# Performance work log

Hardware: AMD Instinct MI355X
Metric: run time of the kernel (lower is better)

## Reference

```python
import jax, jax.numpy as jnp
import numpy as np

B, S, D = 4, 2048, 768
H = 12
HD = D // H  # 64


def setup_inputs() -> dict:
    key = jax.random.key(0)
    k1, k2, k3 = jax.random.split(key, 3)
    x = jax.random.normal(k1, (B, S, D), dtype=jnp.float32)
    w_qkv = jax.random.normal(k2, (D, 3 * D), dtype=jnp.float32) * (1.0 / np.sqrt(D))
    b_qkv = jnp.zeros((3 * D,), dtype=jnp.float32)
    w_proj = jax.random.normal(k3, (D, D), dtype=jnp.float32) * (1.0 / np.sqrt(D))
    b_proj = jnp.zeros((D,), dtype=jnp.float32)
    return {"x": x, "w_qkv": w_qkv, "b_qkv": b_qkv, "w_proj": w_proj, "b_proj": b_proj}


def reference(x, w_qkv, b_qkv, w_proj, b_proj):
    b, s, d = x.shape
    qkv = x @ w_qkv + b_qkv                      # [B,S,3D]
    q, k, v = jnp.split(qkv, 3, axis=-1)
    # [B,S,D] -> [B,H,S,HD]
    q = q.reshape(b, s, H, HD).transpose(0, 2, 1, 3)
    k = k.reshape(b, s, H, HD).transpose(0, 2, 1, 3)
    v = v.reshape(b, s, H, HD).transpose(0, 2, 1, 3)
    scores = jnp.einsum("bhqd,bhkd->bhqk", q, k) / jnp.sqrt(jnp.float32(HD))
    causal = jnp.tril(jnp.ones((s, s), dtype=bool))
    scores = jnp.where(causal[None, None, :, :], scores, jnp.float32(-jnp.inf))
    attn = jax.nn.softmax(scores, axis=-1)       # dropout p=0.0 -> identity
    out = jnp.einsum("bhqk,bhkd->bhqd", attn, v)  # [B,H,S,HD]
    out = out.transpose(0, 2, 1, 3).reshape(b, s, d)
    return out @ w_proj + b_proj
```

## Files before the change

kernel.cpp:

```cpp
#include <hip/hip_runtime.h>
#include <hip/hip_bf16.h>

typedef __hip_bfloat16 bf16;
typedef __bf16 bf16x8 __attribute__((ext_vector_type(8)));
typedef float f32x4 __attribute__((ext_vector_type(4)));

#define MFMA(a, b, c) __builtin_amdgcn_mfma_f32_16x16x32_bf16(a, b, c, 0, 0, 0)
#define EXP2F(x) __builtin_exp2f(x)

constexpr int Bn = 4, Sn = 2048, Dn = 768, Hn = 12;
constexpr int N3 = 3 * Dn;
constexpr int Mrows = Bn * Sn;

constexpr size_t XB_OFF    = 0;
constexpr size_t WQKV_OFF  = 12582912;
constexpr size_t WPROJ_OFF = 16121856;
constexpr size_t Q_OFF     = 17301504;
constexpr size_t K_OFF     = 29884416;
constexpr size_t VT_OFF    = 42467328;
constexpr size_t O_OFF     = 55050240;

#define QSCALE 0.1803368801111243f

__device__ __forceinline__ void gload16(const void* g, void* l) {
  __builtin_amdgcn_global_load_lds((__attribute__((address_space(1))) void*)g,
                                   (__attribute__((address_space(3))) void*)l,
                                   16, 0, 0);
}

__device__ __forceinline__ unsigned int cvt_pk_bf16(float lo, float hi) {
  unsigned int r;
  asm("v_cvt_pk_bf16_f32 %0, %1, %2" : "=v"(r) : "v"(lo), "v"(hi));
  return r;
}

__global__ __launch_bounds__(256) void cvt_x_kernel(const float* __restrict__ in,
                                                    bf16* __restrict__ out, int n4) {
  int i = blockIdx.x * 256 + threadIdx.x;
  if (i >= n4) return;
  float4 f = reinterpret_cast<const float4*>(in)[i];
  uint2 o;
  o.x = cvt_pk_bf16(f.x, f.y);
  o.y = cvt_pk_bf16(f.z, f.w);
  reinterpret_cast<uint2*>(out)[i] = o;
}

__global__ __launch_bounds__(256) void transpose_cvt(const float* __restrict__ in,
                                                     bf16* __restrict__ out, int K, int N) {
  __shared__ float tile[32][33];
  int n0 = blockIdx.x * 32, k0 = blockIdx.y * 32;
  int tx = threadIdx.x & 31, ty = threadIdx.x >> 5;
  for (int r = ty; r < 32; r += 8)
    tile[r][tx] = in[(size_t)(k0 + r) * N + n0 + tx];
  __syncthreads();
  for (int r = ty; r < 32; r += 8)
    out[(size_t)(n0 + r) * K + k0 + tx] = __float2bfloat16(tile[tx][r]);
}

__global__ __launch_bounds__(256) void gemm_qkv(const bf16* __restrict__ A,
                                                const bf16* __restrict__ BT,
                                                const float* __restrict__ bias,
                                                bf16* __restrict__ Qo,
                                                bf16* __restrict__ Ko,
                                                bf16* __restrict__ Vt) {
  __shared__ __align__(16) bf16 As[2][128 * 32];
  __shared__ __align__(16) bf16 Bs[2][128 * 32];
  const int tid = threadIdx.x;
  const int m0 = blockIdx.x * 128, n0 = blockIdx.y * 128;
  const int w = tid >> 6, lane = tid & 63;
  const int wr = w >> 1, wc = w & 1;
  const int lr = lane & 15, lg = lane >> 4;

  f32x4 acc[4][4] = {};

  auto stage = [&](int k0, int sb) {
    for (int r = 0; r < 2; ++r) {
      int c = tid + r * 256;
      int row = c >> 2, ch = c & 3;
      int gch = ch ^ ((row >> 1) & 3);
      gload16(A + (size_t)(m0 + row) * Dn + k0 + gch * 8, &As[sb][c * 8]);
      gload16(BT + (size_t)(n0 + row) * Dn + k0 + gch * 8, &Bs[sb][c * 8]);
    }
  };

  stage(0, 0);
  __syncthreads();

  const int sw = (lr >> 1) & 3;
  const int aoff = (wr * 64 + lr) * 32 + ((lg ^ sw) << 3);
  const int boff = (wc * 64 + lr) * 32 + ((lg ^ sw) << 3);
  int buf = 0;

  for (int kt = 0; kt < 24; ++kt) {
    if (kt < 23) stage((kt + 1) * 32, buf ^ 1);
    bf16x8 af[4], bfr[4];
    for (int mi = 0; mi < 4; ++mi)
      af[mi] = *reinterpret_cast<const bf16x8*>(&As[buf][aoff + mi * 512]);
    for (int ni = 0; ni < 4; ++ni)
      bfr[ni] = *reinterpret_cast<const bf16x8*>(&Bs[buf][boff + ni * 512]);
    for (int mi = 0; mi < 4; ++mi)
      for (int ni = 0; ni < 4; ++ni)
        acc[mi][ni] = MFMA(af[mi], bfr[ni], acc[mi][ni]);
    __syncthreads();
    buf ^= 1;
  }

  for (int ni = 0; ni < 4; ++ni) {
    const int col = n0 + wc * 64 + ni * 16 + lr;
    const float bv = bias[col];
    const int seg = (col >= Dn) + (col >= 2 * Dn);
    const int d = col - seg * Dn;
    const int h = d >> 6, hd = d & 63;
    for (int mi = 0; mi < 4; ++mi) {
      f32x4 v = acc[mi][ni];
      const int row0 = m0 + wr * 64 + mi * 16 + lg * 4;
      const int b = row0 >> 11, s0 = row0 & 2047;
      const size_t bh = (size_t)(b * Hn + h);
      if (seg == 2) {
        uint2 pk;
        pk.x = cvt_pk_bf16(v[0] + bv, v[1] + bv);
        pk.y = cvt_pk_bf16(v[2] + bv, v[3] + bv);
        *reinterpret_cast<uint2*>(&Vt[(bh * 64 + hd) * Sn + s0]) = pk;
      } else if (seg == 0) {
        for (int r = 0; r < 4; ++r)
          Qo[(bh * Sn + s0 + r) * 64 + hd] = __float2bfloat16((v[r] + bv) * QSCALE);
      } else {
        for (int r = 0; r < 4; ++r)
          Ko[(bh * Sn + s0 + r) * 64 + hd] = __float2bfloat16(v[r] + bv);
      }
    }
  }
}

__global__ __launch_bounds__(512) void attn_fwd(const bf16* __restrict__ Q,
                                                const bf16* __restrict__ K,
                                                const bf16* __restrict__ Vt,
                                                bf16* __restrict__ O) {
  __shared__ __align__(16) bf16 Ks[2][64 * 64];
  __shared__ __align__(16) bf16 Vs[2][64 * 64];
  __shared__ __align__(16) bf16 Ps[8][16 * 64];
  const int tid = threadIdx.x, w = tid >> 6, lane = tid & 63;
  const int lr = lane & 15, lg = lane >> 4;
  const int bid = blockIdx.x;
  const int pt = bid / 48;
  const int qt = (pt < 8) ? (15 - 2 * pt) : (2 * pt - 16);
  const int bh = bid % 48;
  const int q0 = qt * 128;
  const size_t base = (size_t)bh * Sn * 64;
  const int wrow = q0 + w * 16;

  bf16x8 qf[2];
  for (int kk = 0; kk < 2; ++kk)
    qf[kk] = *reinterpret_cast<const bf16x8*>(
        Q + base + (size_t)(wrow + lr) * 64 + kk * 32 + lg * 8);

  f32x4 o[4] = {};
  f32x4 lacc = {};

  const int nt = 2 * qt + 2;

  const int r0 = tid >> 3, s0w = (tid & 7) ^ (r0 & 7);
  const bf16* kp = K + base + r0 * 64 + s0w * 8;
  const bf16* vp = Vt + base + (size_t)r0 * Sn + s0w * 8;

  gload16(kp, &Ks[0][tid * 8]);
  gload16(vp, &Vs[0][tid * 8]);
  kp += 4096; vp += 64;
  __syncthreads();

  int buf = 0;
  for (int t = 0; t < nt; ++t) {
    if (t + 1 < nt) {
      const int sb = buf ^ 1;
      gload16(kp, &Ks[sb][tid * 8]);
      gload16(vp, &Vs[sb][tid * 8]);
      kp += 4096; vp += 64;
    }

    if (t * 64 <= wrow + 15) {
      f32x4 sf[4];
      __builtin_amdgcn_s_setprio(1);
      for (int ni = 0; ni < 4; ++ni) {
        const int krow = ni * 16 + lr;
        bf16x8 kf0 = *reinterpret_cast<const bf16x8*>(&Ks[buf][krow * 64 + (lg ^ (lr & 7)) * 8]);
        bf16x8 kf1 = *reinterpret_cast<const bf16x8*>(&Ks[buf][krow * 64 + ((4 + lg) ^ (lr & 7)) * 8]);
        f32x4 z = {};
        z = MFMA(kf0, qf[0], z);
        z = MFMA(kf1, qf[1], z);
        sf[ni] = z;
      }
      __builtin_amdgcn_s_setprio(0);
      if (t * 64 + 63 > wrow) {
        const int qg = wrow + lr;
        for (int ni = 0; ni < 4; ++ni)
          for (int r = 0; r < 4; ++r) {
            int kg = t * 64 + ni * 16 + lg * 4 + r;
            if (kg > qg) sf[ni][r] = -1e30f;
          }
      }
      for (int ni = 0; ni < 4; ++ni) {
        f32x4 z = sf[ni];
        z[0] = EXP2F(z[0]);
        z[1] = EXP2F(z[1]);
        z[2] = EXP2F(z[2]);
        z[3] = EXP2F(z[3]);
        sf[ni] = z;
        lacc += z;
      }
      for (int ni = 0; ni < 4; ++ni) {
        const int chunk = ni * 2 + (lg >> 1);
        const int eoff = lr * 64 + ((chunk ^ (lr & 7)) << 3) + ((lg & 1) << 2);
        uint2 pk;
        pk.x = cvt_pk_bf16(sf[ni][0], sf[ni][1]);
        pk.y = cvt_pk_bf16(sf[ni][2], sf[ni][3]);
        *reinterpret_cast<uint2*>(&Ps[w][eoff]) = pk;
      }
      asm volatile("s_waitcnt lgkmcnt(0)" ::: "memory");
      __builtin_amdgcn_sched_barrier(0);
      __builtin_amdgcn_s_setprio(1);
      for (int kk = 0; kk < 2; ++kk) {
        const int psw = ((kk * 4 + lg) ^ (lr & 7)) << 3;
        bf16x8 pf = *reinterpret_cast<const bf16x8*>(&Ps[w][lr * 64 + psw]);
        for (int di = 0; di < 4; ++di) {
          bf16x8 vf = *reinterpret_cast<const bf16x8*>(&Vs[buf][(di * 16 + lr) * 64 + psw]);
          o[di] = MFMA(vf, pf, o[di]);
        }
      }
      __builtin_amdgcn_s_setprio(0);
    }
    __syncthreads();
    buf ^= 1;
  }

  float l = (lacc[0] + lacc[1]) + (lacc[2] + lacc[3]);
  l += __shfl_xor(l, 16);
  l += __shfl_xor(l, 32);
  const float inv = 1.0f / l;
  const int b = bh / Hn, h = bh % Hn;
  const size_t rowbase = ((size_t)b * Sn + wrow + lr) * Dn + h * 64;
  for (int di = 0; di < 4; ++di) {
    f32x4 ov = o[di];
    uint2 pk;
    pk.x = cvt_pk_bf16(ov[0] * inv, ov[1] * inv);
    pk.y = cvt_pk_bf16(ov[2] * inv, ov[3] * inv);
    *reinterpret_cast<uint2*>(&O[rowbase + di * 16 + lg * 4]) = pk;
  }
}

__global__ __launch_bounds__(256) void gemm_proj(const bf16* __restrict__ A,
                                                 const bf16* __restrict__ BT,
                                                 const float* __restrict__ bias,
                                                 float* __restrict__ out) {
  __shared__ __align__(16) bf16 As[2][128 * 32];
  __shared__ __align__(16) bf16 Bs[2][128 * 32];
  const int tid = threadIdx.x;
  const int m0 = blockIdx.x * 128, n0 = blockIdx.y * 128;
  const int w = tid >> 6, lane = tid & 63;
  const int wr = w >> 1, wc = w & 1;
  const int lr = lane & 15, lg = lane >> 4;

  f32x4 acc[4][4] = {};

  auto stage = [&](int k0, int sb) {
    for (int r = 0; r < 2; ++r) {
      int c = tid + r * 256;
      int row = c >> 2, ch = c & 3;
      int gch = ch ^ ((row >> 1) & 3);
      gload16(A + (size_t)(m0 + row) * Dn + k0 + gch * 8, &As[sb][c * 8]);
      gload16(BT + (size_t)(n0 + row) * Dn + k0 + gch * 8, &Bs[sb][c * 8]);
    }
  };

  stage(0, 0);
  __syncthreads();

  const int sw = (lr >> 1) & 3;
  const int aoff = (wr * 64 + lr) * 32 + ((lg ^ sw) << 3);
  const int boff = (wc * 64 + lr) * 32 + ((lg ^ sw) << 3);
  int buf = 0;

  for (int kt = 0; kt < 24; ++kt) {
    if (kt < 23) stage((kt + 1) * 32, buf ^ 1);
    bf16x8 af[4], bfr[4];
    for (int mi = 0; mi < 4; ++mi)
      af[mi] = *reinterpret_cast<const bf16x8*>(&As[buf][aoff + mi * 512]);
    for (int ni = 0; ni < 4; ++ni)
      bfr[ni] = *reinterpret_cast<const bf16x8*>(&Bs[buf][boff + ni * 512]);
    for (int mi = 0; mi < 4; ++mi)
      for (int ni = 0; ni < 4; ++ni)
        acc[mi][ni] = MFMA(af[mi], bfr[ni], acc[mi][ni]);
    __syncthreads();
    buf ^= 1;
  }

  for (int ni = 0; ni < 4; ++ni) {
    const int col = n0 + wc * 64 + ni * 16 + lr;
    const float bv = bias[col];
    for (int mi = 0; mi < 4; ++mi) {
      f32x4 v = acc[mi][ni];
      for (int r = 0; r < 4; ++r) {
        const int row = m0 + wr * 64 + mi * 16 + lg * 4 + r;
        out[(size_t)row * Dn + col] = v[r] + bv;
      }
    }
  }
}

extern "C" void kernel_launch(void* const* d_in, const int* in_sizes, int n_in,
                              void* d_out, int out_size, void* d_ws, size_t ws_size,
                              hipStream_t stream) {
  const float* x      = (const float*)d_in[0];
  const float* w_qkv  = (const float*)d_in[1];
  const float* b_qkv  = (const float*)d_in[2];
  const float* w_proj = (const float*)d_in[3];
  const float* b_proj = (const float*)d_in[4];
  float* out = (float*)d_out;

  char* ws = (char*)d_ws;
  bf16* xb     = (bf16*)(ws + XB_OFF);
  bf16* wqkvT  = (bf16*)(ws + WQKV_OFF);
  bf16* wprojT = (bf16*)(ws + WPROJ_OFF);
  bf16* Qb     = (bf16*)(ws + Q_OFF);
  bf16* Kb     = (bf16*)(ws + K_OFF);
  bf16* Vtb    = (bf16*)(ws + VT_OFF);
  bf16* Ob     = (bf16*)(ws + O_OFF);

  cvt_x_kernel<<<(Mrows * Dn / 4 + 255) / 256, 256, 0, stream>>>(x, xb, Mrows * Dn / 4);
  transpose_cvt<<<dim3(N3 / 32, Dn / 32), 256, 0, stream>>>(w_qkv, wqkvT, Dn, N3);
  transpose_cvt<<<dim3(Dn / 32, Dn / 32), 256, 0, stream>>>(w_proj, wprojT, Dn, Dn);
  gemm_qkv<<<dim3(Mrows / 128, N3 / 128), 256, 0, stream>>>(xb, wqkvT, b_qkv, Qb, Kb, Vtb);
  attn_fwd<<<768, 512, 0, stream>>>(Qb, Kb, Vtb, Ob);
  gemm_proj<<<dim3(Mrows / 128, Dn / 128), 256, 0, stream>>>(Ob, wprojT, b_proj, out);
}
```

Baseline: 160.7 us.

## Shrink attention blocks to 32 query rows with 2 waves each

Reworks the attention kernel so each block covers 32 query rows with two wavefronts instead of 128 rows with eight. The grid grows to 3072 blocks, scheduled heaviest-first, and each thread loads four K/V chunks per tile. The per-wave causal skip is dropped because the tile count now matches each block's diagonal, and the mask is applied only on the last tile. This is meant to cut wasted work and load imbalance on causal tiles and to raise occupancy. In exchange, each K/V tile is loaded from global memory by four times as many blocks, so reuse drops and memory traffic rises.

```diff
diff --git a/kernel.cpp b/kernel.cpp
--- a/kernel.cpp
+++ b/kernel.cpp
@@ -132,20 +132,19 @@
   }
 }
 
-__global__ __launch_bounds__(512) void attn_fwd(const bf16* __restrict__ Q,
+__global__ __launch_bounds__(128) void attn_fwd(const bf16* __restrict__ Q,
                                                 const bf16* __restrict__ K,
                                                 const bf16* __restrict__ Vt,
                                                 bf16* __restrict__ O) {
   __shared__ __align__(16) bf16 Ks[2][64 * 64];
   __shared__ __align__(16) bf16 Vs[2][64 * 64];
-  __shared__ __align__(16) bf16 Ps[8][16 * 64];
+  __shared__ __align__(16) bf16 Ps[2][16 * 64];
   const int tid = threadIdx.x, w = tid >> 6, lane = tid & 63;
   const int lr = lane & 15, lg = lane >> 4;
   const int bid = blockIdx.x;
-  const int pt = bid / 48;
-  const int qt = (pt < 8) ? (15 - 2 * pt) : (2 * pt - 16);
+  const int qidx = 63 - (bid / 48);
   const int bh = bid % 48;
-  const int q0 = qt * 128;
+  const int q0 = qidx * 32;
   const size_t base = (size_t)bh * Sn * 64;
   const int wrow = q0 + w * 16;
 
@@ -157,77 +156,86 @@
   f32x4 o[4] = {};
   f32x4 lacc = {};
 
-  const int nt = 2 * qt + 2;
-
-  const int r0 = tid >> 3, s0w = (tid & 7) ^ (r0 & 7);
-  const bf16* kp = K + base + r0 * 64 + s0w * 8;
-  const bf16* vp = Vt + base + (size_t)r0 * Sn + s0w * 8;
-
-  gload16(kp, &Ks[0][tid * 8]);
-  gload16(vp, &Vs[0][tid * 8]);
-  kp += 4096; vp += 64;
+  const int nt = (q0 >> 6) + 1;
+
+  const bf16* kp[4];
+  const bf16* vp[4];
+#pragma unroll
+  for (int j = 0; j < 4; ++j) {
+    const int p = tid + j * 128;
+    const int row = p >> 3, sc = (p & 7) ^ (row & 7);
+    kp[j] = K + base + row * 64 + sc * 8;
+    vp[j] = Vt + base + (size_t)row * Sn + sc * 8;
+  }
+#pragma unroll
+  for (int j = 0; j < 4; ++j) {
+    gload16(kp[j], &Ks[0][(tid + j * 128) * 8]);
+    gload16(vp[j], &Vs[0][(tid + j * 128) * 8]);
+    kp[j] += 4096; vp[j] += 64;
+  }
   __syncthreads();
 
   int buf = 0;
   for (int t = 0; t < nt; ++t) {
     if (t + 1 < nt) {
       const int sb = buf ^ 1;
-      gload16(kp, &Ks[sb][tid * 8]);
-      gload16(vp, &Vs[sb][tid * 8]);
-      kp += 4096; vp += 64;
-    }
-
-    if (t * 64 <= wrow + 15) {
-      f32x4 sf[4];
-      __builtin_amdgcn_s_setprio(1);
-      for (int ni = 0; ni < 4; ++ni) {
-        const int krow = ni * 16 + lr;
-        bf16x8 kf0 = *reinterpret_cast<const bf16x8*>(&Ks[buf][krow * 64 + (lg ^ (lr & 7)) * 8]);
-        bf16x8 kf1 = *reinterpret_cast<const bf16x8*>(&Ks[buf][krow * 64 + ((4 + lg) ^ (lr & 7)) * 8]);
-        f32x4 z = {};
-        z = MFMA(kf0, qf[0], z);
-        z = MFMA(kf1, qf[1], z);
-        sf[ni] = z;
+#pragma unroll
+      for (int j = 0; j < 4; ++j) {
+        gload16(kp[j], &Ks[sb][(tid + j * 128) * 8]);
+        gload16(vp[j], &Vs[sb][(tid + j * 128) * 8]);
+        kp[j] += 4096; vp[j] += 64;
       }
-      __builtin_amdgcn_s_setprio(0);
-      if (t * 64 + 63 > wrow) {
-        const int qg = wrow + lr;
-        for (int ni = 0; ni < 4; ++ni)
-          for (int r = 0; r < 4; ++r) {
-            int kg = t * 64 + ni * 16 + lg * 4 + r;
-            if (kg > qg) sf[ni][r] = -1e30f;
-          }
+    }
+
+    f32x4 sf[4];
+    __builtin_amdgcn_s_setprio(1);
+    for (int ni = 0; ni < 4; ++ni) {
+      const int krow = ni * 16 + lr;
+      bf16x8 kf0 = *reinterpret_cast<const bf16x8*>(&Ks[buf][krow * 64 + (lg ^ (lr & 7)) * 8]);
+      bf16x8 kf1 = *reinterpret_cast<const bf16x8*>(&Ks[buf][krow * 64 + ((4 + lg) ^ (lr & 7)) * 8]);
+      f32x4 z = {};
+      z = MFMA(kf0, qf[0], z);
+      z = MFMA(kf1, qf[1], z);
+      sf[ni] = z;
+    }
+    __builtin_amdgcn_s_setprio(0);
+    if (t == nt - 1) {
+      const int qg = wrow + lr;
+      for (int ni = 0; ni < 4; ++ni)
+        for (int r = 0; r < 4; ++r) {
+          int kg = t * 64 + ni * 16 + lg * 4 + r;
+          if (kg > qg) sf[ni][r] = -1e30f;
+        }
+    }
+    for (int ni = 0; ni < 4; ++ni) {
+      f32x4 z = sf[ni];
+      z[0] = EXP2F(z[0]);
+      z[1] = EXP2F(z[1]);
+      z[2] = EXP2F(z[2]);
+      z[3] = EXP2F(z[3]);
+      sf[ni] = z;
+      lacc += z;
+    }
+    for (int ni = 0; ni < 4; ++ni) {
+      const int chunk = ni * 2 + (lg >> 1);
+      const int eoff = lr * 64 + ((chunk ^ (lr & 7)) << 3) + ((lg & 1) << 2);
+      uint2 pk;
+      pk.x = cvt_pk_bf16(sf[ni][0], sf[ni][1]);
+      pk.y = cvt_pk_bf16(sf[ni][2], sf[ni][3]);
+      *reinterpret_cast<uint2*>(&Ps[w][eoff]) = pk;
+    }
+    asm volatile("s_waitcnt lgkmcnt(0)" ::: "memory");
+    __builtin_amdgcn_sched_barrier(0);
+    __builtin_amdgcn_s_setprio(1);
+    for (int kk = 0; kk < 2; ++kk) {
+      const int psw = ((kk * 4 + lg) ^ (lr & 7)) << 3;
+      bf16x8 pf = *reinterpret_cast<const bf16x8*>(&Ps[w][lr * 64 + psw]);
+      for (int di = 0; di < 4; ++di) {
+        bf16x8 vf = *reinterpret_cast<const bf16x8*>(&Vs[buf][(di * 16 + lr) * 64 + psw]);
+        o[di] = MFMA(vf, pf, o[di]);
       }
-      for (int ni = 0; ni < 4; ++ni) {
-        f32x4 z = sf[ni];
-        z[0] = EXP2F(z[0]);
-        z[1] = EXP2F(z[1]);
-        z[2] = EXP2F(z[2]);
-        z[3] = EXP2F(z[3]);
-        sf[ni] = z;
-        lacc += z;
-      }
-      for (int ni = 0; ni < 4; ++ni) {
-        const int chunk = ni * 2 + (lg >> 1);
-        const int eoff = lr * 64 + ((chunk ^ (lr & 7)) << 3) + ((lg & 1) << 2);
-        uint2 pk;
-        pk.x = cvt_pk_bf16(sf[ni][0], sf[ni][1]);
-        pk.y = cvt_pk_bf16(sf[ni][2], sf[ni][3]);
-        *reinterpret_cast<uint2*>(&Ps[w][eoff]) = pk;
-      }
-      asm volatile("s_waitcnt lgkmcnt(0)" ::: "memory");
-      __builtin_amdgcn_sched_barrier(0);
-      __builtin_amdgcn_s_setprio(1);
-      for (int kk = 0; kk < 2; ++kk) {
-        const int psw = ((kk * 4 + lg) ^ (lr & 7)) << 3;
-        bf16x8 pf = *reinterpret_cast<const bf16x8*>(&Ps[w][lr * 64 + psw]);
-        for (int di = 0; di < 4; ++di) {
-          bf16x8 vf = *reinterpret_cast<const bf16x8*>(&Vs[buf][(di * 16 + lr) * 64 + psw]);
-          o[di] = MFMA(vf, pf, o[di]);
-        }
-      }
-      __builtin_amdgcn_s_setprio(0);
-    }
+    }
+    __builtin_amdgcn_s_setprio(0);
     __syncthreads();
     buf ^= 1;
   }
@@ -329,6 +337,6 @@
   transpose_cvt<<<dim3(N3 / 32, Dn / 32), 256, 0, stream>>>(w_qkv, wqkvT, Dn, N3);
   transpose_cvt<<<dim3(Dn / 32, Dn / 32), 256, 0, stream>>>(w_proj, wprojT, Dn, Dn);
   gemm_qkv<<<dim3(Mrows / 128, N3 / 128), 256, 0, stream>>>(xb, wqkvT, b_qkv, Qb, Kb, Vtb);
-  attn_fwd<<<768, 512, 0, stream>>>(Qb, Kb, Vtb, Ob);
+  attn_fwd<<<64 * 48, 128, 0, stream>>>(Qb, Kb, Vtb, Ob);
   gemm_proj<<<dim3(Mrows / 128, Dn / 128), 256, 0, stream>>>(Ob, wprojT, b_proj, out);
 }
```

After: 157.0 us. 2.3% less time.
